# Kernel optimization log

Hardware: AMD Instinct MI355X
Metric: run time of the kernel (lower is better)

The kernel has to match this reference:

```python
import jax, jax.numpy as jnp
import numpy as np


def _conv(x, w):
    # NCHW cross-correlation, stride 1, zero 'SAME' padding (kernel//2 each side)
    return jax.lax.conv_general_dilated(x, w, window_strides=(1, 1), padding='SAME',
                                        dimension_numbers=('NCHW', 'OIHW', 'NCHW'))


def _conv_t(y, w):
    # adjoint of _conv(x, w): spatially flipped kernel with in/out channels swapped
    wt = jnp.transpose(jnp.flip(w, (2, 3)), (1, 0, 2, 3))
    return _conv(y, wt)


def _spline(x, coefs, x_min, x_max):
    # uniform-knot linear spline with linear extrapolation (clamp=False)
    K = coefs.shape[-1]
    step = (x_max - x_min) / (K - 1)
    t = (x - x_min) / step
    idx = jnp.clip(jnp.floor(t), 0, K - 2).astype(jnp.int32)
    frac = t - idx
    if coefs.shape[0] == 1:
        c = coefs[0]
        c0, c1v = c[idx], c[idx + 1]
    else:
        ch = jnp.arange(coefs.shape[0]).reshape(1, -1, 1, 1)
        c0, c1v = coefs[ch, idx], coefs[ch, idx + 1]
    return c0 * (1.0 - frac) + c1v * frac


def _forward(y, sigma, w1_0, w1_1, w1_2, m1_0, m1_1, m1_2, m2_w, m3_w,
             c_sp1, c_sp2, c_sp3, c_lam, c_scal, n_out, n_in):
    LC = m2_w.shape[0]  # last_c = 128
    lmbda = _spline(sigma, c_lam, -1.0, 51.0)              # (B,1,1,1)
    sig_e = sigma * jnp.ones((1, LC, 1, 1), sigma.dtype)   # (B,LC,1,1)
    scaling = jnp.exp(_spline(sig_e, c_scal, -1.0, 51.0)) / (sig_e + 1e-5)

    def W1(x):
        return _conv(_conv(_conv(x, w1_0), w1_1), w1_2)

    def W1t(v):
        return _conv_t(_conv_t(_conv_t(v, w1_2), w1_1), w1_0)

    def cal_mask(x):
        t = _spline(jnp.abs(_conv(_conv(_conv(x, m1_0), m1_1), m1_2)), c_sp1, 0.0, 3.0)
        t = _spline(jnp.abs(_conv(t, m2_w)), c_sp2, 0.0, 3.0)
        t = _conv(t, m3_w)
        t = _spline(scaling * jnp.abs(t), c_sp3, 0.0, 3.0)  # last_act
        return jnp.clip(t, 0.01, 1.0)

    def BtB(x, mask):
        # (x + lmbda * Lt(L(x))) / (1 + lmbda) with L(x)=W1(x)*mask, Lt(v)=W1t(v*mask)
        return (x + lmbda * W1t(W1(x) * mask * mask)) / (1.0 + lmbda)

    eps_in = 1e-6

    def cg(bb, x0, mask):
        # masked-batch CG: converged images (r_norm <= eps) get alpha=beta=0,
        # mathematically identical to the torch code's dynamic batch shrinking
        b = bb / (1.0 + lmbda)
        r0 = b - BtB(x0, mask)
        rn0 = jnp.sum(r0 * r0, axis=(1, 2, 3), keepdims=True)

        def step(carry, _):
            x, r, p, rn = carry
            act = rn > eps_in
            Bp = BtB(p, mask)
            denom = jnp.sum(p * Bp, axis=(1, 2, 3), keepdims=True)
            alpha = jnp.where(act, rn / jnp.where(act, denom, 1.0), 0.0)
            x = x + alpha * p
            r2 = r - alpha * Bp
            rn2 = jnp.sum(r2 * r2, axis=(1, 2, 3), keepdims=True)
            beta = jnp.where(act, rn2 / jnp.where(act, rn, 1.0), 0.0)
            return (x, r2, r2 + beta * p, rn2), None

        (x, _, _, _), _ = jax.lax.scan(step, (x0, r0, r0, rn0), None, length=n_in)
        return x

    # eval-mode denoise: outer mask-recompute loop around inner CG solves
    c_k = jnp.zeros_like(y)
    c_k_old = c_k
    for _ in range(n_out):
        mask = cal_mask(c_k)
        c_k = cg(y, c_k_old, mask)
        c_k_old = c_k
    return c_k


def setup_inputs() -> dict:
    key = jax.random.key(0)
    ks = jax.random.split(key, 10)
    B, H, W = 8, 128, 128
    y = jax.random.normal(ks[0], (B, 1, H, W), jnp.float32)
    sigma = jax.random.uniform(ks[1], (B, 1, 1, 1), jnp.float32) * 0.2 + 0.05

    def cw(k, co, ci, ksz):
        return jax.random.normal(k, (co, ci, ksz, ksz), jnp.float32) / np.float32(np.sqrt(ci * ksz * ksz))

    w1_0 = cw(ks[2], 4, 1, 9); w1_1 = cw(ks[3], 8, 4, 9); w1_2 = cw(ks[4], 128, 8, 9)
    m1_0 = cw(ks[5], 4, 1, 9); m1_1 = cw(ks[6], 8, 4, 9); m1_2 = cw(ks[7], 128, 8, 9)
    m2_w = cw(ks[8], 128, 128, 3); m3_w = cw(ks[9], 128, 128, 3)
    c_sp1 = jnp.linspace(0.0, 3.0, 31).astype(jnp.float32).reshape(1, 31)   # identity init
    c_sp2 = jnp.linspace(0.0, 3.0, 31).astype(jnp.float32).reshape(1, 31)   # identity init
    g = jnp.linspace(0.0, 3.0, 31).astype(jnp.float32)
    c_sp3 = jnp.exp(-(g - 1.5) ** 2).reshape(1, 31)                          # gaussian init
    c_lam = jnp.linspace(-1.0, 51.0, 53).astype(jnp.float32).reshape(1, 53)  # identity init
    c_scal = 3.0 * jnp.ones((128, 14), jnp.float32)                          # constant 3.0 init
    return {"y": y, "sigma": sigma,
            "w1_0": w1_0, "w1_1": w1_1, "w1_2": w1_2,
            "m1_0": m1_0, "m1_1": m1_1, "m1_2": m1_2,
            "m2_w": m2_w, "m3_w": m3_w,
            "c_sp1": c_sp1, "c_sp2": c_sp2, "c_sp3": c_sp3,
            "c_lam": c_lam, "c_scal": c_scal,
            "n_out": 2, "n_in": 6}


def reference(y, sigma, w1_0, w1_1, w1_2, m1_0, m1_1, m1_2, m2_w, m3_w,
              c_sp1, c_sp2, c_sp3, c_lam, c_scal, n_out, n_in):
    return _forward(y, sigma, w1_0, w1_1, w1_2, m1_0, m1_1, m1_2, m2_w, m3_w,
                    c_sp1, c_sp2, c_sp3, c_lam, c_scal, n_out, n_in)
```

## Files before the change

kernel.cpp:

```cpp
#include <hip/hip_runtime.h>

#define HW 16384
#define BATCH 8

typedef unsigned short u16;
typedef __attribute__((ext_vector_type(8))) short bfrag;
typedef __attribute__((ext_vector_type(4))) float ffrag;
typedef __attribute__((ext_vector_type(4))) float f4v;

__device__ __forceinline__ u16 f2bf(float f) {
  unsigned int u = __float_as_uint(f);
  u += 0x7FFFu + ((u >> 16) & 1u);
  return (u16)(u >> 16);
}
__device__ __forceinline__ float bf2f(u16 h) {
  return __uint_as_float(((unsigned int)h) << 16);
}
__device__ __forceinline__ ffrag mfma16(bfrag a, bfrag b, ffrag c) {
  return __builtin_amdgcn_mfma_f32_16x16x32_bf16(a, b, c, 0, 0, 0);
}

__device__ __forceinline__ float spline_eval(float x, const float* __restrict__ c,
                                             int K, float xmin, float xmax) {
  float step = (xmax - xmin) / (float)(K - 1);
  float t = (x - xmin) / step;
  float fidx = floorf(t);
  fidx = fminf(fmaxf(fidx, 0.0f), (float)(K - 2));
  int idx = (int)fidx;
  float frac = t - fidx;
  return c[idx] * (1.0f - frac) + c[idx + 1] * frac;
}
__device__ __forceinline__ float spline31(float x, const float* __restrict__ c) {
  float t = x * 10.0f;
  float fi = floorf(t);
  fi = fminf(fmaxf(fi, 0.0f), 29.0f);
  int i = (int)fi;
  float fr = t - fi;
  return c[i] * (1.0f - fr) + c[i + 1] * fr;
}

template<int KS, int CIW, int CO, int NTT, int NSLICE, int TAPS, int CHUNKS, bool TR>
__global__ void k_prepw(const float* __restrict__ W, u16* __restrict__ hi,
                        u16* __restrict__ lo) {
  int gid = blockIdx.x * 256 + threadIdx.x;
  const int total = NSLICE * CHUNKS * NTT * 64;
  if (gid >= total) return;
  int L = gid & 63;
  int rest = gid >> 6;
  int ntg = rest % NTT; rest /= NTT;
  int ch = rest % CHUNKS;
  int sl = rest / CHUNKS;
  int q = L >> 4, n = L & 15;
  int tap = ch * 4 + q;
  int co = ntg * 16 + n;
  int dh = tap / KS, dw = tap - dh * KS;
  for (int j = 0; j < 8; ++j) {
    int ci = sl * 8 + j;
    float v = 0.0f;
    if (tap < TAPS && co < CO) {
      if (TR)
        v = W[(((size_t)ci * CO + co) * KS + (KS - 1 - dh)) * KS + (KS - 1 - dw)];
      else
        v = W[(((size_t)co * CIW + ci) * KS + dh) * KS + dw];
    }
    u16 h = f2bf(v);
    hi[(size_t)gid * 8 + j] = h;
    lo[(size_t)gid * 8 + j] = f2bf(v - bf2f(h));
  }
}

template<int KS, int SLICES, int TAPS, int CHUNKS, int NT, int NTT, int EPI>
__global__ __launch_bounds__(256) void bconv(
    const u16* __restrict__ in, const u16* __restrict__ wHi,
    float* __restrict__ outF, u16* __restrict__ outBf,
    const u16* __restrict__ mskc)
{
  constexpr int P  = KS / 2;
  constexpr int IW = 16 + 2 * P;
  constexpr int IH = 16 + 2 * P;

  __shared__ __align__(16) u16 sA[IH * IW * 8];

  const int tid = threadIdx.x;
  const int wv  = tid >> 6;
  const int L   = tid & 63;
  const int q   = L >> 4;
  const int n16 = L & 15;

  const int tx = blockIdx.x & 7, ty = blockIdx.x >> 3;
  const int w0 = tx * 16, h0 = ty * 16;
  const int bb = blockIdx.y;
  const int bz = blockIdx.z;

  ffrag acc[4][NT];
#pragma unroll
  for (int i = 0; i < 4; ++i)
#pragma unroll
    for (int t = 0; t < NT; ++t) acc[i][t] = (ffrag)0.0f;

  for (int slc = 0; slc < SLICES; ++slc) {
    __syncthreads();
    for (int e = tid; e < IH * IW; e += 256) {
      int ih = e / IW, iw = e - ih * IW;
      int gh = h0 + ih - P, gw = w0 + iw - P;
      f4v v = (f4v)0.0f;
      if (gh >= 0 && gh < 128 && gw >= 0 && gw < 128)
        v = *(const f4v*)(in + (((size_t)(bb * SLICES + slc) * HW) + gh * 128 + gw) * 8);
      *(f4v*)(sA + (size_t)e * 8) = v;
    }
    __syncthreads();

    const u16* wS = wHi + (size_t)slc * CHUNKS * NTT * 512;
    for (int ch = 0; ch < CHUNKS; ++ch) {
      int tap = ch * 4 + q;
      int dh = 0, dw = 0;
      if (tap < TAPS) { dh = tap / KS; dw = tap - dh * KS; }
      int toff = dh * IW + dw;
      bfrag A[4];
#pragma unroll
      for (int i = 0; i < 4; ++i)
        A[i] = *(const bfrag*)(sA + ((wv * 4 + i) * IW + n16 + toff) * 8);
#pragma unroll
      for (int t = 0; t < NT; ++t) {
        bfrag B = *(const bfrag*)(wS + ((size_t)ch * NTT + bz * NT + t) * 512 + L * 8);
#pragma unroll
        for (int i = 0; i < 4; ++i) acc[i][t] = mfma16(A[i], B, acc[i][t]);
      }
    }
  }

#pragma unroll
  for (int i = 0; i < 4; ++i) {
    const int h = h0 + wv * 4 + i;
#pragma unroll
    for (int t = 0; t < NT; ++t) {
      const int co = bz * (NT * 16) + t * 16 + n16;
#pragma unroll
      for (int r = 0; r < 4; ++r) {
        const int w = w0 + q * 4 + r;
        float v = acc[i][t][r];
        if (EPI == 0) {
          if (n16 < 8)
            outF[(((size_t)bb * 8 + n16) * 128 + h) * 128 + w] = v;
        } else if (EPI == 3) {
          size_t o = (((size_t)(bb * 16 + (co >> 3)) * HW) + h * 128 + w) * 8 + (co & 7);
          float m = bf2f(mskc[o]);
          outBf[o] = f2bf(v * m * m);
        }
      }
    }
  }
}

template<int KS, int CIN, int NSLICE, int TAPS, int CHUNKS,
         int TH, int MTW, int NT, int NTT, int EPI>
__global__ __launch_bounds__(256) void mconv(
    const float* __restrict__ inF,
    const u16* __restrict__ wHi, const u16* __restrict__ wLo,
    float* __restrict__ outF, u16* __restrict__ outBf,
    const float* __restrict__ sp, const float* __restrict__ sl,
    int binOfs, int boutOfs)
{
  constexpr int P  = KS / 2;
  constexpr int IW = 16 + 2 * P;
  constexpr int IH = TH + 2 * P;

  __shared__ __align__(16) u16 sHi[IH * IW * 8];
  __shared__ __align__(16) u16 sLo[IH * IW * 8];

  const int tid = threadIdx.x;
  const int wv  = tid >> 6;
  const int L   = tid & 63;
  const int q   = L >> 4;
  const int n16 = L & 15;

  const int tx = blockIdx.x & 7;
  const int ty = blockIdx.x >> 3;
  const int w0 = tx * 16, h0 = ty * TH;
  const int bin  = (int)blockIdx.y + binOfs;
  const int bout = (int)blockIdx.y + boutOfs;
  const int bz = blockIdx.z;

  ffrag acc[MTW][NT];
#pragma unroll
  for (int i = 0; i < MTW; ++i)
#pragma unroll
    for (int t = 0; t < NT; ++t) acc[i][t] = (ffrag)0.0f;

  for (int slc = 0; slc < NSLICE; ++slc) {
    __syncthreads();
    for (int e = tid; e < IH * IW; e += 256) {
      int ih = e / IW, iw = e - ih * IW;
      int gh = h0 + ih - P, gw = w0 + iw - P;
      float v[8];
      if (gh >= 0 && gh < 128 && gw >= 0 && gw < 128) {
        const float* s = inF + (((size_t)(bin * 128 + gh) * 128 + gw) * CIN + slc * 8);
        f4v a = *(const f4v*)s;
        f4v b2 = *(const f4v*)(s + 4);
        v[0] = a[0]; v[1] = a[1]; v[2] = a[2]; v[3] = a[3];
        v[4] = b2[0]; v[5] = b2[1]; v[6] = b2[2]; v[7] = b2[3];
      } else {
#pragma unroll
        for (int j = 0; j < 8; ++j) v[j] = 0.0f;
      }
#pragma unroll
      for (int j = 0; j < 8; ++j) {
        u16 hb = f2bf(v[j]);
        sHi[e * 8 + j] = hb;
        sLo[e * 8 + j] = f2bf(v[j] - bf2f(hb));
      }
    }
    __syncthreads();

    const u16* wHs = wHi + (size_t)slc * CHUNKS * NTT * 512;
    const u16* wLs = wLo + (size_t)slc * CHUNKS * NTT * 512;
    for (int ch = 0; ch < CHUNKS; ++ch) {
      int tap = ch * 4 + q;
      int dh = tap / KS;
      int dw = tap - dh * KS;
      int toff = (tap < TAPS) ? (dh * IW + dw) : 0;
      bfrag Ah[MTW], Al[MTW];
#pragma unroll
      for (int i = 0; i < MTW; ++i) {
        int a8 = ((wv * MTW + i) * IW + n16 + toff) * 8;
        Ah[i] = *(const bfrag*)(sHi + a8);
        Al[i] = *(const bfrag*)(sLo + a8);
      }
#pragma unroll
      for (int t = 0; t < NT; ++t) {
        size_t off = ((size_t)ch * NTT + bz * NT + t) * 512 + L * 8;
        bfrag Bh = *(const bfrag*)(wHs + off);
        bfrag Bl = *(const bfrag*)(wLs + off);
#pragma unroll
        for (int i = 0; i < MTW; ++i) {
          acc[i][t] = mfma16(Ah[i], Bh, acc[i][t]);
          acc[i][t] = mfma16(Ah[i], Bl, acc[i][t]);
          acc[i][t] = mfma16(Al[i], Bh, acc[i][t]);
        }
      }
    }
  }

#pragma unroll
  for (int i = 0; i < MTW; ++i) {
    const int h = h0 + wv * MTW + i;
#pragma unroll
    for (int t = 0; t < NT; ++t) {
      const int co = bz * (NT * 16) + t * 16 + n16;
#pragma unroll
      for (int r = 0; r < 4; ++r) {
        const int w = w0 + q * 4 + r;
        float v = acc[i][t][r];
        if (EPI == 1) {
          outF[(((size_t)bout * 128 + h) * 128 + w) * 128 + co] = spline31(fabsf(v), sp);
        } else if (EPI == 2) {
          float s = sl[bout * 128 + co];
          float x = spline31(s * fabsf(v), sp);
          x = fminf(fmaxf(x, 0.01f), 1.0f);
          size_t o = (((size_t)(bout * 16 + (co >> 3)) * HW) + h * 128 + w) * 8 + (co & 7);
          outBf[o] = f2bf(x);
        }
      }
    }
  }
}

template<int OUT>
__global__ __launch_bounds__(256) void fused_fwd(
    const float* __restrict__ in, const float* __restrict__ wA,
    const float* __restrict__ wB, float* __restrict__ outF,
    u16* __restrict__ outBf)
{
  __shared__ float sX[32 * 48];
  __shared__ float sT4[4][24 * 41];
  __shared__ float sWA[81 * 4];
  __shared__ float sWB[4 * 81 * 8];

  const int tid = threadIdx.x;
  const int b   = blockIdx.z;
  const int h0  = (blockIdx.x >> 2) * 16;
  const int w0  = (blockIdx.x & 3) * 32;

  for (int e = tid; e < 32 * 48; e += 256) {
    int r = e / 48, c = e - r * 48;
    int gh = h0 - 8 + r, gw = w0 - 8 + c;
    float v = 0.0f;
    if (gh >= 0 && gh < 128 && gw >= 0 && gw < 128)
      v = in[(size_t)b * HW + gh * 128 + gw];
    sX[e] = v;
  }
  for (int e = tid; e < 324; e += 256) {
    int co = e & 3, tap = e >> 2;
    sWA[tap * 4 + co] = wA[co * 81 + tap];
  }
  for (int e = tid; e < 2592; e += 256) {
    int co = e & 7;
    int rest = e >> 3;
    int tap = rest % 81, ci = rest / 81;
    sWB[(ci * 81 + tap) * 8 + co] = wB[((size_t)co * 4 + ci) * 81 + tap];
  }
  __syncthreads();

  for (int e = tid; e < 960; e += 256) {
    int r = e / 40, c = e - r * 40;
    int gh = h0 - 4 + r, gw = w0 - 4 + c;
    float a0 = 0.0f, a1 = 0.0f, a2 = 0.0f, a3 = 0.0f;
    if (gh >= 0 && gh < 128 && gw >= 0 && gw < 128) {
      for (int kh = 0; kh < 9; ++kh) {
#pragma unroll
        for (int kw = 0; kw < 9; ++kw) {
          float x = sX[(r + kh) * 48 + (c + kw)];
          const float* wp = &sWA[(kh * 9 + kw) * 4];
          a0 += x * wp[0]; a1 += x * wp[1]; a2 += x * wp[2]; a3 += x * wp[3];
        }
      }
    }
    sT4[0][r * 41 + c] = a0;
    sT4[1][r * 41 + c] = a1;
    sT4[2][r * 41 + c] = a2;
    sT4[3][r * 41 + c] = a3;
  }
  __syncthreads();

  const int c  = tid & 31;
  const int r0 = tid >> 5;
  float acc[2][8];
#pragma unroll
  for (int j = 0; j < 2; ++j)
#pragma unroll
    for (int co = 0; co < 8; ++co) acc[j][co] = 0.0f;

  for (int ci = 0; ci < 4; ++ci) {
    const float* t4c = sT4[ci];
    for (int kh = 0; kh < 9; ++kh) {
#pragma unroll
      for (int kw = 0; kw < 9; ++kw) {
        float x0 = t4c[(r0 + kh) * 41 + c + kw];
        float x1 = t4c[(r0 + 8 + kh) * 41 + c + kw];
        const float* wp = &sWB[(ci * 81 + kh * 9 + kw) * 8];
#pragma unroll
        for (int co = 0; co < 8; ++co) {
          acc[0][co] += x0 * wp[co];
          acc[1][co] += x1 * wp[co];
        }
      }
    }
  }

#pragma unroll
  for (int j = 0; j < 2; ++j) {
    const int h = h0 + r0 + 8 * j;
    const int w = w0 + c;
#pragma unroll
    for (int co = 0; co < 8; ++co) {
      float v = acc[j][co];
      if (OUT == 0)
        outF[(((size_t)b * 128 + h) * 128 + w) * 8 + co] = v;
      else
        outBf[((size_t)b * HW + h * 128 + w) * 8 + co] = f2bf(v);
    }
  }
}

template<int KS, int CI, int CO, int CIC, int COT, int TH, int EPI, bool TR>
__global__ __launch_bounds__(256) void conv_k(
    const float* __restrict__ in, const float* __restrict__ wt,
    float* __restrict__ out, const float* __restrict__ aux,
    const float* __restrict__ sl)
{
  constexpr int P  = KS / 2;
  constexpr int TW = 32;
  constexpr int IH = TH + 2 * P;
  constexpr int IW = TW + 2 * P;
  constexpr int RPT = TH / 8;
  constexpr int NCH = CI / CIC;
  static_assert(CIC * NCH == CI, "channel split mismatch");

  __shared__ float sIn[CIC * IH * IW];
  __shared__ float sW[CIC * KS * KS * COT];

  const int tid = threadIdx.x;
  const int nTW = 128 / TW;
  const int th0 = (blockIdx.x / nTW) * TH;
  const int tw0 = (blockIdx.x % nTW) * TW;
  const int b   = blockIdx.z;

  float acc[RPT][COT];
#pragma unroll
  for (int j = 0; j < RPT; ++j)
#pragma unroll
    for (int co = 0; co < COT; ++co) acc[j][co] = 0.0f;

  const int c  = tid & 31;
  const int r0 = tid >> 5;

  for (int ch = 0; ch < NCH; ++ch) {
    const int ci0 = ch * CIC;
    __syncthreads();
    for (int e = tid; e < CIC * IH * IW; e += 256) {
      int ci  = e / (IH * IW);
      int rem = e - ci * (IH * IW);
      int ih  = rem / IW;
      int iw  = rem - ih * IW;
      int gh = th0 + ih - P, gw = tw0 + iw - P;
      float v = 0.0f;
      if (gh >= 0 && gh < 128 && gw >= 0 && gw < 128)
        v = in[((size_t)(b * CI + ci0 + ci) * 128 + gh) * 128 + gw];
      sIn[e] = v;
    }
    for (int e = tid; e < CIC * KS * KS * COT; e += 256) {
      int co = e & (COT - 1);
      int k  = e / COT;
      int ci = k / (KS * KS);
      int kk = k - ci * (KS * KS);
      int kh = kk / KS, kw = kk - kh * KS;
      float wv;
      if (!TR)
        wv = wt[(((size_t)co * CI + ci0 + ci) * KS + kh) * KS + kw];
      else
        wv = wt[(((size_t)(ci0 + ci) * CO + co) * KS + (KS - 1 - kh)) * KS + (KS - 1 - kw)];
      sW[e] = wv;
    }
    __syncthreads();

    for (int ci = 0; ci < CIC; ++ci) {
      for (int kh = 0; kh < KS; ++kh) {
        const float* inb = &sIn[(ci * IH + r0 + kh) * IW + c];
        const float* wb  = &sW[(ci * KS + kh) * KS * COT];
#pragma unroll
        for (int kw = 0; kw < KS; ++kw) {
          float xv[RPT];
#pragma unroll
          for (int j = 0; j < RPT; ++j) xv[j] = inb[8 * j * IW + kw];
#pragma unroll
          for (int co = 0; co < COT; ++co) {
            float wv = wb[kw * COT + co];
#pragma unroll
            for (int j = 0; j < RPT; ++j) acc[j][co] += xv[j] * wv;
          }
        }
      }
    }
  }

#pragma unroll
  for (int j = 0; j < RPT; ++j) {
    const int h = th0 + r0 + 8 * j;
    const int w = tw0 + c;
#pragma unroll
    for (int co = 0; co < COT; ++co) {
      float v = acc[j][co];
      if (EPI == 5) {
        size_t o = ((size_t)b * 128 + h) * 128 + w;
        float l = sl[b];
        out[o] = (aux[o] + l * v) / (1.0f + l);
      } else {
        out[((size_t)(b * CO + co) * 128 + h) * 128 + w] = v;
      }
    }
  }
}

__global__ void k_scalars(const float* __restrict__ sigma, const float* __restrict__ c_lam,
                          const float* __restrict__ c_scal, float* __restrict__ lam,
                          float* __restrict__ scal) {
  int tid = threadIdx.x;
  if (tid < BATCH) lam[tid] = spline_eval(sigma[tid], c_lam, 53, -1.0f, 51.0f);
  for (int j = tid; j < BATCH * 128; j += 256) {
    int b = j >> 7, chn = j & 127;
    float s = sigma[b];
    scal[j] = expf(spline_eval(s, c_scal + chn * 14, 14, -1.0f, 51.0f)) / (s + 1e-5f);
  }
}

__global__ void k_binit(const float* __restrict__ y, const float* __restrict__ lam,
                        float* __restrict__ bimg, float* __restrict__ x) {
  int i = blockIdx.x * 256 + threadIdx.x;
  int b = i >> 14;
  bimg[i] = y[i] / (1.0f + lam[b]);
  x[i] = 0.0f;
}

__global__ void k_rinit(const float* __restrict__ bimg, const float* __restrict__ Bp,
                        float* __restrict__ r, float* __restrict__ p) {
  int i = blockIdx.x * 256 + threadIdx.x;
  float v = bimg[i] - Bp[i];
  r[i] = v;
  p[i] = v;
}

__global__ void k_dot(const float* __restrict__ a, const float* __restrict__ bv,
                      float* __restrict__ out) {
  __shared__ float s[256];
  int b = blockIdx.x;
  float sum = 0.0f;
  for (int i = threadIdx.x; i < HW; i += 256) sum += a[b * HW + i] * bv[b * HW + i];
  s[threadIdx.x] = sum;
  __syncthreads();
  for (int st = 128; st > 0; st >>= 1) {
    if (threadIdx.x < st) s[threadIdx.x] += s[threadIdx.x + st];
    __syncthreads();
  }
  if (threadIdx.x == 0) out[b] = s[0];
}

__global__ void k_update_xr(float* __restrict__ x, float* __restrict__ r,
                            const float* __restrict__ p, const float* __restrict__ Bp,
                            const float* __restrict__ rn, const float* __restrict__ den) {
  int i = blockIdx.x * 256 + threadIdx.x;
  int b = i >> 14;
  float rnb = rn[b];
  float alpha = rnb > 1e-6f ? rnb / den[b] : 0.0f;
  x[i] += alpha * p[i];
  r[i] -= alpha * Bp[i];
}

__global__ void k_update_p(float* __restrict__ p, const float* __restrict__ r,
                           const float* __restrict__ rnOld, const float* __restrict__ rnNew) {
  int i = blockIdx.x * 256 + threadIdx.x;
  int b = i >> 14;
  float ro = rnOld[b];
  float beta = ro > 1e-6f ? rnNew[b] / ro : 0.0f;
  p[i] = r[i] + beta * p[i];
}

__global__ void k_copy(const float* __restrict__ x, float* __restrict__ out) {
  int i = blockIdx.x * 256 + threadIdx.x;
  out[i] = x[i];
}

extern "C" void kernel_launch(void* const* d_in, const int* in_sizes, int n_in_,
                              void* d_out, int out_size, void* d_ws, size_t ws_size,
                              hipStream_t stream) {
  const float* y      = (const float*)d_in[0];
  const float* sigma  = (const float*)d_in[1];
  const float* w1_0   = (const float*)d_in[2];
  const float* w1_1   = (const float*)d_in[3];
  const float* w1_2   = (const float*)d_in[4];
  const float* m1_0   = (const float*)d_in[5];
  const float* m1_1   = (const float*)d_in[6];
  const float* m1_2   = (const float*)d_in[7];
  const float* m2_w   = (const float*)d_in[8];
  const float* m3_w   = (const float*)d_in[9];
  const float* c_sp1  = (const float*)d_in[10];
  const float* c_sp2  = (const float*)d_in[11];
  const float* c_sp3  = (const float*)d_in[12];
  const float* c_lam  = (const float*)d_in[13];
  const float* c_scal = (const float*)d_in[14];

  char* cur = (char*)d_ws;
  auto alloc = [&](size_t bytes) {
    char* p = cur;
    cur += (bytes + 255) & ~(size_t)255;
    return p;
  };

  u16* wA_hi  = (u16*)alloc(86016 * 2);
  u16* wA_lo  = (u16*)alloc(86016 * 2);
  u16* wAm_hi = (u16*)alloc(86016 * 2);
  u16* wAm_lo = (u16*)alloc(86016 * 2);
  u16* wB_hi  = (u16*)alloc(172032 * 2);
  u16* wB_lo  = (u16*)alloc(172032 * 2);
  u16* wC2_hi = (u16*)alloc(196608 * 2);
  u16* wC2_lo = (u16*)alloc(196608 * 2);
  u16* wC3_hi = (u16*)alloc(196608 * 2);
  u16* wC3_lo = (u16*)alloc(196608 * 2);

  char* region1 = alloc((size_t)16777216 * 4);
  float* P1f    = (float*)region1;
  u16*   big2c  = (u16*)region1;
  u16* mask_c = (u16*)alloc((size_t)16777216 * 2);
  char* region2 = alloc((size_t)4 * 128 * 128 * 128 * 4);
  float* P2s = (float*)region2;
  float* t8n = (float*)region2;
  float* t4  = (float*)(region2 + 4194304);
  char* region3 = alloc((size_t)1048576 * 4);
  float* t8f = (float*)region3;
  u16*   t8c = (u16*)region3;

  float* bimg = (float*)alloc(131072 * 4);
  float* xbuf = (float*)alloc(131072 * 4);
  float* rbuf = (float*)alloc(131072 * 4);
  float* pbuf = (float*)alloc(131072 * 4);
  float* Bp   = (float*)alloc(131072 * 4);
  float* lam  = (float*)alloc(8 * 4);
  float* scal = (float*)alloc(1024 * 4);
  float* rnA  = (float*)alloc(8 * 4);
  float* rnB  = (float*)alloc(8 * 4);
  float* den  = (float*)alloc(8 * 4);

  const dim3 blk(256);

  k_prepw<9, 8, 128, 8, 1, 81, 21, false><<<dim3(42), blk, 0, stream>>>(w1_2, wA_hi, wA_lo);
  k_prepw<9, 8, 128, 8, 1, 81, 21, false><<<dim3(42), blk, 0, stream>>>(m1_2, wAm_hi, wAm_lo);
  k_prepw<9, 8, 8, 1, 16, 81, 21, true><<<dim3(84), blk, 0, stream>>>(w1_2, wB_hi, wB_lo);
  k_prepw<3, 128, 128, 8, 16, 9, 3, false><<<dim3(96), blk, 0, stream>>>(m2_w, wC2_hi, wC2_lo);
  k_prepw<3, 128, 128, 8, 16, 9, 3, false><<<dim3(96), blk, 0, stream>>>(m3_w, wC3_hi, wC3_lo);

  k_scalars<<<dim3(1), blk, 0, stream>>>(sigma, c_lam, c_scal, lam, scal);
  k_binit<<<dim3(512), blk, 0, stream>>>(y, lam, bimg, xbuf);

  auto BtB = [&](const float* vin, float* vout) {
    fused_fwd<1><<<dim3(32, 1, 8), blk, 0, stream>>>(vin, w1_0, w1_1, nullptr, t8c);
    bconv<9, 1, 81, 21, 2, 8, 3><<<dim3(64, 8, 4), blk, 0, stream>>>(
        t8c, wA_hi, nullptr, big2c, mask_c);
    bconv<9, 16, 81, 21, 1, 1, 0><<<dim3(64, 8, 1), blk, 0, stream>>>(
        big2c, wB_hi, t8n, nullptr, nullptr);
    conv_k<9, 8, 4, 2, 4, 16, 0, true><<<dim3(32, 1, 8), blk, 0, stream>>>(
        t8n, w1_1, t4, nullptr, nullptr);
    conv_k<9, 4, 1, 1, 1, 16, 5, true><<<dim3(32, 1, 8), blk, 0, stream>>>(
        t4, w1_0, vout, vin, lam);
  };

  for (int outer = 0; outer < 2; ++outer) {
    fused_fwd<0><<<dim3(32, 1, 8), blk, 0, stream>>>(xbuf, m1_0, m1_1, t8f, nullptr);
    mconv<9, 8, 1, 81, 21, 16, 4, 2, 8, 1><<<dim3(64, 8, 4), blk, 0, stream>>>(
        t8f, wAm_hi, wAm_lo, P1f, nullptr, c_sp1, nullptr, 0, 0);
    for (int bc = 0; bc < 2; ++bc) {
      mconv<3, 128, 16, 9, 3, 16, 4, 2, 8, 1><<<dim3(64, 4, 4), blk, 0, stream>>>(
          P1f, wC2_hi, wC2_lo, P2s, nullptr, c_sp2, nullptr, bc * 4, 0);
      mconv<3, 128, 16, 9, 3, 16, 4, 2, 8, 2><<<dim3(64, 4, 4), blk, 0, stream>>>(
          P2s, wC3_hi, wC3_lo, nullptr, mask_c, c_sp3, scal, 0, bc * 4);
    }

    BtB(xbuf, Bp);
    k_rinit<<<dim3(512), blk, 0, stream>>>(bimg, Bp, rbuf, pbuf);
    k_dot<<<dim3(8), blk, 0, stream>>>(rbuf, rbuf, rnA);

    float* rA = rnA;
    float* rB = rnB;
    for (int it = 0; it < 6; ++it) {
      BtB(pbuf, Bp);
      k_dot<<<dim3(8), blk, 0, stream>>>(pbuf, Bp, den);
      k_update_xr<<<dim3(512), blk, 0, stream>>>(xbuf, rbuf, pbuf, Bp, rA, den);
      k_dot<<<dim3(8), blk, 0, stream>>>(rbuf, rbuf, rB);
      k_update_p<<<dim3(512), blk, 0, stream>>>(pbuf, rbuf, rA, rB);
      float* tmp = rA; rA = rB; rB = tmp;
    }
  }

  k_copy<<<dim3(512), blk, 0, stream>>>(xbuf, (float*)d_out);
}
```

Measured before the change: 3.433 ms.

## Fuse transposed conv tail and CG vector updates into fewer kernels

Replaces the two fp32 transposed 9x9 conv kernels (8->4 and 4->1 channels) with a single fused_tail kernel. It keeps the 4-channel intermediate, with halo, in shared memory and applies the lambda blend in its epilogue. The preceding bconv now writes a bf16 channel-interleaved 8-channel output instead of fp32 planar, which halves that traffic but adds bf16 rounding. The CG residual init, x/r update, norm and p update are merged into per-image kernels with in-block reductions. This cuts launches and global round trips, but those kernels now run on only 8 blocks, and fused_tail recomputes the halo region.

```diff
diff --git a/kernel.cpp b/kernel.cpp
--- a/kernel.cpp
+++ b/kernel.cpp
@@ -72,8 +72,7 @@
 template<int KS, int SLICES, int TAPS, int CHUNKS, int NT, int NTT, int EPI>
 __global__ __launch_bounds__(256) void bconv(
     const u16* __restrict__ in, const u16* __restrict__ wHi,
-    float* __restrict__ outF, u16* __restrict__ outBf,
-    const u16* __restrict__ mskc)
+    u16* __restrict__ outBf, const u16* __restrict__ mskc)
 {
   constexpr int P  = KS / 2;
   constexpr int IW = 16 + 2 * P;
@@ -139,9 +138,9 @@
       for (int r = 0; r < 4; ++r) {
         const int w = w0 + q * 4 + r;
         float v = acc[i][t][r];
-        if (EPI == 0) {
+        if (EPI == 4) {
           if (n16 < 8)
-            outF[(((size_t)bb * 8 + n16) * 128 + h) * 128 + w] = v;
+            outBf[((size_t)bb * HW + h * 128 + w) * 8 + n16] = f2bf(v);
         } else if (EPI == 3) {
           size_t o = (((size_t)(bb * 16 + (co >> 3)) * HW) + h * 128 + w) * 8 + (co & 7);
           float m = bf2f(mskc[o]);
@@ -362,102 +361,92 @@
   }
 }
 
-template<int KS, int CI, int CO, int CIC, int COT, int TH, int EPI, bool TR>
-__global__ __launch_bounds__(256) void conv_k(
-    const float* __restrict__ in, const float* __restrict__ wt,
-    float* __restrict__ out, const float* __restrict__ aux,
-    const float* __restrict__ sl)
+__global__ __launch_bounds__(256) void fused_tail(
+    const u16* __restrict__ t8v, const float* __restrict__ w11,
+    const float* __restrict__ w10, const float* __restrict__ vin,
+    const float* __restrict__ lam, float* __restrict__ vout)
 {
-  constexpr int P  = KS / 2;
-  constexpr int TW = 32;
-  constexpr int IH = TH + 2 * P;
-  constexpr int IW = TW + 2 * P;
-  constexpr int RPT = TH / 8;
-  constexpr int NCH = CI / CIC;
-  static_assert(CIC * NCH == CI, "channel split mismatch");
-
-  __shared__ float sIn[CIC * IH * IW];
-  __shared__ float sW[CIC * KS * KS * COT];
+  __shared__ float sX[8][32 * 33];
+  __shared__ float sT4[4][24 * 25];
+  __shared__ float sW1[8 * 81 * 4];
+  __shared__ float sW0[4 * 81];
 
   const int tid = threadIdx.x;
-  const int nTW = 128 / TW;
-  const int th0 = (blockIdx.x / nTW) * TH;
-  const int tw0 = (blockIdx.x % nTW) * TW;
   const int b   = blockIdx.z;
-
-  float acc[RPT][COT];
-#pragma unroll
-  for (int j = 0; j < RPT; ++j)
-#pragma unroll
-    for (int co = 0; co < COT; ++co) acc[j][co] = 0.0f;
-
-  const int c  = tid & 31;
-  const int r0 = tid >> 5;
-
-  for (int ch = 0; ch < NCH; ++ch) {
-    const int ci0 = ch * CIC;
-    __syncthreads();
-    for (int e = tid; e < CIC * IH * IW; e += 256) {
-      int ci  = e / (IH * IW);
-      int rem = e - ci * (IH * IW);
-      int ih  = rem / IW;
-      int iw  = rem - ih * IW;
-      int gh = th0 + ih - P, gw = tw0 + iw - P;
-      float v = 0.0f;
-      if (gh >= 0 && gh < 128 && gw >= 0 && gw < 128)
-        v = in[((size_t)(b * CI + ci0 + ci) * 128 + gh) * 128 + gw];
-      sIn[e] = v;
-    }
-    for (int e = tid; e < CIC * KS * KS * COT; e += 256) {
-      int co = e & (COT - 1);
-      int k  = e / COT;
-      int ci = k / (KS * KS);
-      int kk = k - ci * (KS * KS);
-      int kh = kk / KS, kw = kk - kh * KS;
-      float wv;
-      if (!TR)
-        wv = wt[(((size_t)co * CI + ci0 + ci) * KS + kh) * KS + kw];
-      else
-        wv = wt[(((size_t)(ci0 + ci) * CO + co) * KS + (KS - 1 - kh)) * KS + (KS - 1 - kw)];
-      sW[e] = wv;
-    }
-    __syncthreads();
-
-    for (int ci = 0; ci < CIC; ++ci) {
-      for (int kh = 0; kh < KS; ++kh) {
-        const float* inb = &sIn[(ci * IH + r0 + kh) * IW + c];
-        const float* wb  = &sW[(ci * KS + kh) * KS * COT];
-#pragma unroll
-        for (int kw = 0; kw < KS; ++kw) {
-          float xv[RPT];
-#pragma unroll
-          for (int j = 0; j < RPT; ++j) xv[j] = inb[8 * j * IW + kw];
-#pragma unroll
-          for (int co = 0; co < COT; ++co) {
-            float wv = wb[kw * COT + co];
-#pragma unroll
-            for (int j = 0; j < RPT; ++j) acc[j][co] += xv[j] * wv;
+  const int h0  = (blockIdx.x >> 3) * 16;
+  const int w0  = (blockIdx.x & 7) * 16;
+
+  for (int e = tid; e < 1024; e += 256) {
+    int r = e >> 5, c = e & 31;
+    int gh = h0 - 8 + r, gw = w0 - 8 + c;
+    float v[8];
+    if (gh >= 0 && gh < 128 && gw >= 0 && gw < 128) {
+      const u16* s = t8v + ((size_t)b * HW + gh * 128 + gw) * 8;
+#pragma unroll
+      for (int ci = 0; ci < 8; ++ci) v[ci] = bf2f(s[ci]);
+    } else {
+#pragma unroll
+      for (int ci = 0; ci < 8; ++ci) v[ci] = 0.0f;
+    }
+#pragma unroll
+    for (int ci = 0; ci < 8; ++ci) sX[ci][r * 33 + c] = v[ci];
+  }
+  for (int e = tid; e < 2592; e += 256) {
+    int co = e & 3;
+    int rest = e >> 2;
+    int tap = rest % 81, ci = rest / 81;
+    sW1[(ci * 81 + tap) * 4 + co] = w11[(size_t)(ci * 4 + co) * 81 + (80 - tap)];
+  }
+  for (int e = tid; e < 324; e += 256) {
+    int tap = e % 81, ci = e / 81;
+    sW0[ci * 81 + tap] = w10[(size_t)ci * 81 + (80 - tap)];
+  }
+  __syncthreads();
+
+  for (int e = tid; e < 288; e += 256) {
+    int r = e / 12, c2 = (e - r * 12) * 2;
+    int gh = h0 - 4 + r;
+    int gw0 = w0 - 4 + c2;
+    float a0[4] = {0, 0, 0, 0}, a1[4] = {0, 0, 0, 0};
+    for (int ci = 0; ci < 8; ++ci) {
+      for (int kh = 0; kh < 9; ++kh) {
+        const float* xb = &sX[ci][(r + kh) * 33 + c2];
+#pragma unroll
+        for (int kw = 0; kw < 9; ++kw) {
+          float x0 = xb[kw], x1 = xb[kw + 1];
+          const float* wp = &sW1[(ci * 81 + kh * 9 + kw) * 4];
+#pragma unroll
+          for (int co = 0; co < 4; ++co) {
+            a0[co] += x0 * wp[co];
+            a1[co] += x1 * wp[co];
           }
         }
       }
     }
-  }
-
-#pragma unroll
-  for (int j = 0; j < RPT; ++j) {
-    const int h = th0 + r0 + 8 * j;
-    const int w = tw0 + c;
-#pragma unroll
-    for (int co = 0; co < COT; ++co) {
-      float v = acc[j][co];
-      if (EPI == 5) {
-        size_t o = ((size_t)b * 128 + h) * 128 + w;
-        float l = sl[b];
-        out[o] = (aux[o] + l * v) / (1.0f + l);
-      } else {
-        out[((size_t)(b * CO + co) * 128 + h) * 128 + w] = v;
-      }
-    }
+    bool in0 = (gh >= 0 && gh < 128 && gw0 >= 0 && gw0 < 128);
+    bool in1 = (gh >= 0 && gh < 128 && (gw0 + 1) >= 0 && (gw0 + 1) < 128);
+#pragma unroll
+    for (int co = 0; co < 4; ++co) {
+      sT4[co][r * 25 + c2]     = in0 ? a0[co] : 0.0f;
+      sT4[co][r * 25 + c2 + 1] = in1 ? a1[co] : 0.0f;
+    }
+  }
+  __syncthreads();
+
+  {
+    int r = tid >> 4, c = tid & 15;
+    float acc = 0.0f;
+    for (int ci = 0; ci < 4; ++ci) {
+      for (int kh = 0; kh < 9; ++kh) {
+        const float* xb = &sT4[ci][(r + kh) * 25 + c];
+        const float* wp = &sW0[ci * 81 + kh * 9];
+#pragma unroll
+        for (int kw = 0; kw < 9; ++kw) acc += xb[kw] * wp[kw];
+      }
+    }
+    size_t o = (size_t)b * HW + (h0 + r) * 128 + (w0 + c);
+    float l = lam[b];
+    vout[o] = (vin[o] + l * acc) / (1.0f + l);
   }
 }
 
@@ -479,14 +468,6 @@
   int b = i >> 14;
   bimg[i] = y[i] / (1.0f + lam[b]);
   x[i] = 0.0f;
-}
-
-__global__ void k_rinit(const float* __restrict__ bimg, const float* __restrict__ Bp,
-                        float* __restrict__ r, float* __restrict__ p) {
-  int i = blockIdx.x * 256 + threadIdx.x;
-  float v = bimg[i] - Bp[i];
-  r[i] = v;
-  p[i] = v;
 }
 
 __global__ void k_dot(const float* __restrict__ a, const float* __restrict__ bv,
@@ -504,24 +485,56 @@
   if (threadIdx.x == 0) out[b] = s[0];
 }
 
-__global__ void k_update_xr(float* __restrict__ x, float* __restrict__ r,
-                            const float* __restrict__ p, const float* __restrict__ Bp,
-                            const float* __restrict__ rn, const float* __restrict__ den) {
-  int i = blockIdx.x * 256 + threadIdx.x;
-  int b = i >> 14;
+__global__ void k_cg0(const float* __restrict__ bimg, const float* __restrict__ Bp,
+                      float* __restrict__ r, float* __restrict__ p,
+                      float* __restrict__ rn) {
+  __shared__ float s[256];
+  int b = blockIdx.x;
+  size_t base = (size_t)b << 14;
+  float local = 0.0f;
+  for (int i = threadIdx.x; i < HW; i += 256) {
+    float v = bimg[base + i] - Bp[base + i];
+    r[base + i] = v;
+    p[base + i] = v;
+    local += v * v;
+  }
+  s[threadIdx.x] = local;
+  __syncthreads();
+  for (int st = 128; st > 0; st >>= 1) {
+    if (threadIdx.x < st) s[threadIdx.x] += s[threadIdx.x + st];
+    __syncthreads();
+  }
+  if (threadIdx.x == 0) rn[b] = s[0];
+}
+
+__global__ void k_cg2(float* __restrict__ x, float* __restrict__ r,
+                      float* __restrict__ p, const float* __restrict__ Bp,
+                      float* __restrict__ rn, const float* __restrict__ den) {
+  __shared__ float s[256];
+  int b = blockIdx.x;
+  size_t base = (size_t)b << 14;
   float rnb = rn[b];
-  float alpha = rnb > 1e-6f ? rnb / den[b] : 0.0f;
-  x[i] += alpha * p[i];
-  r[i] -= alpha * Bp[i];
-}
-
-__global__ void k_update_p(float* __restrict__ p, const float* __restrict__ r,
-                           const float* __restrict__ rnOld, const float* __restrict__ rnNew) {
-  int i = blockIdx.x * 256 + threadIdx.x;
-  int b = i >> 14;
-  float ro = rnOld[b];
-  float beta = ro > 1e-6f ? rnNew[b] / ro : 0.0f;
-  p[i] = r[i] + beta * p[i];
+  bool act = rnb > 1e-6f;
+  float alpha = act ? rnb / den[b] : 0.0f;
+  float local = 0.0f;
+  for (int i = threadIdx.x; i < HW; i += 256) {
+    float pv = p[base + i];
+    x[base + i] += alpha * pv;
+    float rr = r[base + i] - alpha * Bp[base + i];
+    r[base + i] = rr;
+    local += rr * rr;
+  }
+  s[threadIdx.x] = local;
+  __syncthreads();
+  for (int st = 128; st > 0; st >>= 1) {
+    if (threadIdx.x < st) s[threadIdx.x] += s[threadIdx.x + st];
+    __syncthreads();
+  }
+  float rn2 = s[0];
+  float beta = act ? rn2 / rnb : 0.0f;
+  if (threadIdx.x == 0) rn[b] = rn2;
+  for (int i = threadIdx.x; i < HW; i += 256)
+    p[base + i] = r[base + i] + beta * p[base + i];
 }
 
 __global__ void k_copy(const float* __restrict__ x, float* __restrict__ out) {
@@ -567,13 +580,12 @@
   u16* wC3_lo = (u16*)alloc(196608 * 2);
 
   char* region1 = alloc((size_t)16777216 * 4);
-  float* P1f    = (float*)region1;
-  u16*   big2c  = (u16*)region1;
+  float* P1f   = (float*)region1;
+  u16*   big2c = (u16*)region1;
   u16* mask_c = (u16*)alloc((size_t)16777216 * 2);
   char* region2 = alloc((size_t)4 * 128 * 128 * 128 * 4);
   float* P2s = (float*)region2;
-  float* t8n = (float*)region2;
-  float* t4  = (float*)(region2 + 4194304);
+  u16*   t8v = (u16*)region2;
   char* region3 = alloc((size_t)1048576 * 4);
   float* t8f = (float*)region3;
   u16*   t8c = (u16*)region3;
@@ -585,8 +597,7 @@
   float* Bp   = (float*)alloc(131072 * 4);
   float* lam  = (float*)alloc(8 * 4);
   float* scal = (float*)alloc(1024 * 4);
-  float* rnA  = (float*)alloc(8 * 4);
-  float* rnB  = (float*)alloc(8 * 4);
+  float* rn   = (float*)alloc(8 * 4);
   float* den  = (float*)alloc(8 * 4);
 
   const dim3 blk(256);
@@ -603,13 +614,10 @@
   auto BtB = [&](const float* vin, float* vout) {
     fused_fwd<1><<<dim3(32, 1, 8), blk, 0, stream>>>(vin, w1_0, w1_1, nullptr, t8c);
     bconv<9, 1, 81, 21, 2, 8, 3><<<dim3(64, 8, 4), blk, 0, stream>>>(
-        t8c, wA_hi, nullptr, big2c, mask_c);
-    bconv<9, 16, 81, 21, 1, 1, 0><<<dim3(64, 8, 1), blk, 0, stream>>>(
-        big2c, wB_hi, t8n, nullptr, nullptr);
-    conv_k<9, 8, 4, 2, 4, 16, 0, true><<<dim3(32, 1, 8), blk, 0, stream>>>(
-        t8n, w1_1, t4, nullptr, nullptr);
-    conv_k<9, 4, 1, 1, 1, 16, 5, true><<<dim3(32, 1, 8), blk, 0, stream>>>(
-        t4, w1_0, vout, vin, lam);
+        t8c, wA_hi, big2c, mask_c);
+    bconv<9, 16, 81, 21, 1, 1, 4><<<dim3(64, 8, 1), blk, 0, stream>>>(
+        big2c, wB_hi, t8v, nullptr);
+    fused_tail<<<dim3(64, 1, 8), blk, 0, stream>>>(t8v, w1_1, w1_0, vin, lam, vout);
   };
 
   for (int outer = 0; outer < 2; ++outer) {
@@ -624,18 +632,12 @@
     }
 
     BtB(xbuf, Bp);
-    k_rinit<<<dim3(512), blk, 0, stream>>>(bimg, Bp, rbuf, pbuf);
-    k_dot<<<dim3(8), blk, 0, stream>>>(rbuf, rbuf, rnA);
-
-    float* rA = rnA;
-    float* rB = rnB;
+    k_cg0<<<dim3(8), blk, 0, stream>>>(bimg, Bp, rbuf, pbuf, rn);
+
     for (int it = 0; it < 6; ++it) {
       BtB(pbuf, Bp);
       k_dot<<<dim3(8), blk, 0, stream>>>(pbuf, Bp, den);
-      k_update_xr<<<dim3(512), blk, 0, stream>>>(xbuf, rbuf, pbuf, Bp, rA, den);
-      k_dot<<<dim3(8), blk, 0, stream>>>(rbuf, rbuf, rB);
-      k_update_p<<<dim3(512), blk, 0, stream>>>(pbuf, rbuf, rA, rB);
-      float* tmp = rA; rA = rB; rB = tmp;
+      k_cg2<<<dim3(8), blk, 0, stream>>>(xbuf, rbuf, pbuf, Bp, rn, den);
     }
   }
 
```

New measurement: 3.536 ms. 1.03x slower.

## Store mask-path activations as pre-split bf16 hi/lo and fuse CG updates

Applied to the files above, without the earlier changes.

Intermediate activations feeding the MFMA mask convolutions are now written in channel-blocked bf16 hi/lo pairs by the producer epilogues, so the consumer staging loops just copy vectors instead of converting fp32 and splitting per load. Separately, the CG residual init, x/r update, norm reduction and p update are fused into per-batch kernels, removing several launches and the final copy. The fused CG kernels use only one block per image, which reduces parallelism for the elementwise work.

```diff
diff --git a/kernel.cpp b/kernel.cpp
--- a/kernel.cpp
+++ b/kernel.cpp
@@ -155,9 +155,9 @@
 template<int KS, int CIN, int NSLICE, int TAPS, int CHUNKS,
          int TH, int MTW, int NT, int NTT, int EPI>
 __global__ __launch_bounds__(256) void mconv(
-    const float* __restrict__ inF,
+    const u16* __restrict__ inHi, const u16* __restrict__ inLo,
     const u16* __restrict__ wHi, const u16* __restrict__ wLo,
-    float* __restrict__ outF, u16* __restrict__ outBf,
+    u16* __restrict__ outHi, u16* __restrict__ outLo,
     const float* __restrict__ sp, const float* __restrict__ sl,
     int binOfs, int boutOfs)
 {
@@ -192,23 +192,14 @@
     for (int e = tid; e < IH * IW; e += 256) {
       int ih = e / IW, iw = e - ih * IW;
       int gh = h0 + ih - P, gw = w0 + iw - P;
-      float v[8];
+      f4v vh = (f4v)0.0f, vl = (f4v)0.0f;
       if (gh >= 0 && gh < 128 && gw >= 0 && gw < 128) {
-        const float* s = inF + (((size_t)(bin * 128 + gh) * 128 + gw) * CIN + slc * 8);
-        f4v a = *(const f4v*)s;
-        f4v b2 = *(const f4v*)(s + 4);
-        v[0] = a[0]; v[1] = a[1]; v[2] = a[2]; v[3] = a[3];
-        v[4] = b2[0]; v[5] = b2[1]; v[6] = b2[2]; v[7] = b2[3];
-      } else {
-#pragma unroll
-        for (int j = 0; j < 8; ++j) v[j] = 0.0f;
-      }
-#pragma unroll
-      for (int j = 0; j < 8; ++j) {
-        u16 hb = f2bf(v[j]);
-        sHi[e * 8 + j] = hb;
-        sLo[e * 8 + j] = f2bf(v[j] - bf2f(hb));
-      }
+        size_t g = (((size_t)(bin * (CIN / 8) + slc) * HW) + gh * 128 + gw) * 8;
+        vh = *(const f4v*)(inHi + g);
+        vl = *(const f4v*)(inLo + g);
+      }
+      *(f4v*)(sHi + (size_t)e * 8) = vh;
+      *(f4v*)(sLo + (size_t)e * 8) = vl;
     }
     __syncthreads();
 
@@ -251,14 +242,17 @@
       for (int r = 0; r < 4; ++r) {
         const int w = w0 + q * 4 + r;
         float v = acc[i][t][r];
+        size_t o = (((size_t)(bout * 16 + (co >> 3)) * HW) + h * 128 + w) * 8 + (co & 7);
         if (EPI == 1) {
-          outF[(((size_t)bout * 128 + h) * 128 + w) * 128 + co] = spline31(fabsf(v), sp);
+          float x = spline31(fabsf(v), sp);
+          u16 hb = f2bf(x);
+          outHi[o] = hb;
+          outLo[o] = f2bf(x - bf2f(hb));
         } else if (EPI == 2) {
           float s = sl[bout * 128 + co];
           float x = spline31(s * fabsf(v), sp);
           x = fminf(fmaxf(x, 0.01f), 1.0f);
-          size_t o = (((size_t)(bout * 16 + (co >> 3)) * HW) + h * 128 + w) * 8 + (co & 7);
-          outBf[o] = f2bf(x);
+          outHi[o] = f2bf(x);
         }
       }
     }
@@ -268,8 +262,8 @@
 template<int OUT>
 __global__ __launch_bounds__(256) void fused_fwd(
     const float* __restrict__ in, const float* __restrict__ wA,
-    const float* __restrict__ wB, float* __restrict__ outF,
-    u16* __restrict__ outBf)
+    const float* __restrict__ wB, u16* __restrict__ oHi,
+    u16* __restrict__ oLo)
 {
   __shared__ float sX[32 * 48];
   __shared__ float sT4[4][24 * 41];
@@ -354,10 +348,14 @@
 #pragma unroll
     for (int co = 0; co < 8; ++co) {
       float v = acc[j][co];
-      if (OUT == 0)
-        outF[(((size_t)b * 128 + h) * 128 + w) * 8 + co] = v;
-      else
-        outBf[((size_t)b * HW + h * 128 + w) * 8 + co] = f2bf(v);
+      size_t o = ((size_t)b * HW + h * 128 + w) * 8 + co;
+      if (OUT == 0) {
+        u16 hb = f2bf(v);
+        oHi[o] = hb;
+        oLo[o] = f2bf(v - bf2f(hb));
+      } else {
+        oHi[o] = f2bf(v);
+      }
     }
   }
 }
@@ -481,14 +479,6 @@
   x[i] = 0.0f;
 }
 
-__global__ void k_rinit(const float* __restrict__ bimg, const float* __restrict__ Bp,
-                        float* __restrict__ r, float* __restrict__ p) {
-  int i = blockIdx.x * 256 + threadIdx.x;
-  float v = bimg[i] - Bp[i];
-  r[i] = v;
-  p[i] = v;
-}
-
 __global__ void k_dot(const float* __restrict__ a, const float* __restrict__ bv,
                       float* __restrict__ out) {
   __shared__ float s[256];
@@ -504,29 +494,59 @@
   if (threadIdx.x == 0) out[b] = s[0];
 }
 
-__global__ void k_update_xr(float* __restrict__ x, float* __restrict__ r,
-                            const float* __restrict__ p, const float* __restrict__ Bp,
-                            const float* __restrict__ rn, const float* __restrict__ den) {
-  int i = blockIdx.x * 256 + threadIdx.x;
-  int b = i >> 14;
+__global__ void k_cg0(const float* __restrict__ bimg, const float* __restrict__ Bp,
+                      float* __restrict__ r, float* __restrict__ p,
+                      float* __restrict__ rn) {
+  __shared__ float s[256];
+  int b = blockIdx.x;
+  size_t base = (size_t)b << 14;
+  float local = 0.0f;
+  for (int i = threadIdx.x; i < HW; i += 256) {
+    float v = bimg[base + i] - Bp[base + i];
+    r[base + i] = v;
+    p[base + i] = v;
+    local += v * v;
+  }
+  s[threadIdx.x] = local;
+  __syncthreads();
+  for (int st = 128; st > 0; st >>= 1) {
+    if (threadIdx.x < st) s[threadIdx.x] += s[threadIdx.x + st];
+    __syncthreads();
+  }
+  if (threadIdx.x == 0) rn[b] = s[0];
+}
+
+__global__ void k_cg2(float* __restrict__ x, float* __restrict__ r,
+                      float* __restrict__ p, const float* __restrict__ Bp,
+                      float* __restrict__ rn, const float* __restrict__ den,
+                      float* __restrict__ xout) {
+  __shared__ float s[256];
+  int b = blockIdx.x;
+  size_t base = (size_t)b << 14;
   float rnb = rn[b];
-  float alpha = rnb > 1e-6f ? rnb / den[b] : 0.0f;
-  x[i] += alpha * p[i];
-  r[i] -= alpha * Bp[i];
-}
-
-__global__ void k_update_p(float* __restrict__ p, const float* __restrict__ r,
-                           const float* __restrict__ rnOld, const float* __restrict__ rnNew) {
-  int i = blockIdx.x * 256 + threadIdx.x;
-  int b = i >> 14;
-  float ro = rnOld[b];
-  float beta = ro > 1e-6f ? rnNew[b] / ro : 0.0f;
-  p[i] = r[i] + beta * p[i];
-}
-
-__global__ void k_copy(const float* __restrict__ x, float* __restrict__ out) {
-  int i = blockIdx.x * 256 + threadIdx.x;
-  out[i] = x[i];
+  bool act = rnb > 1e-6f;
+  float alpha = act ? rnb / den[b] : 0.0f;
+  float local = 0.0f;
+  for (int i = threadIdx.x; i < HW; i += 256) {
+    float pv = p[base + i];
+    float xv = x[base + i] + alpha * pv;
+    x[base + i] = xv;
+    if (xout) xout[base + i] = xv;
+    float rr = r[base + i] - alpha * Bp[base + i];
+    r[base + i] = rr;
+    local += rr * rr;
+  }
+  s[threadIdx.x] = local;
+  __syncthreads();
+  for (int st = 128; st > 0; st >>= 1) {
+    if (threadIdx.x < st) s[threadIdx.x] += s[threadIdx.x + st];
+    __syncthreads();
+  }
+  float rn2 = s[0];
+  float beta = act ? rn2 / rnb : 0.0f;
+  if (threadIdx.x == 0) rn[b] = rn2;
+  for (int i = threadIdx.x; i < HW; i += 256)
+    p[base + i] = r[base + i] + beta * p[base + i];
 }
 
 extern "C" void kernel_launch(void* const* d_in, const int* in_sizes, int n_in_,
@@ -566,17 +586,20 @@
   u16* wC3_hi = (u16*)alloc(196608 * 2);
   u16* wC3_lo = (u16*)alloc(196608 * 2);
 
-  char* region1 = alloc((size_t)16777216 * 4);
-  float* P1f    = (float*)region1;
-  u16*   big2c  = (u16*)region1;
+  char* region1 = alloc((size_t)16777216 * 2 * 2);
+  u16* P1hi  = (u16*)region1;
+  u16* P1lo  = (u16*)(region1 + (size_t)16777216 * 2);
+  u16* big2c = (u16*)region1;
   u16* mask_c = (u16*)alloc((size_t)16777216 * 2);
-  char* region2 = alloc((size_t)4 * 128 * 128 * 128 * 4);
-  float* P2s = (float*)region2;
+  char* region2 = alloc((size_t)8388608 * 2 * 2);
+  u16* P2hi = (u16*)region2;
+  u16* P2lo = (u16*)(region2 + (size_t)8388608 * 2);
   float* t8n = (float*)region2;
-  float* t4  = (float*)(region2 + 4194304);
-  char* region3 = alloc((size_t)1048576 * 4);
-  float* t8f = (float*)region3;
-  u16*   t8c = (u16*)region3;
+  float* t4  = (float*)(region2 + (size_t)4194304 * 4);
+  char* region3 = alloc((size_t)1048576 * 2 * 2);
+  u16* t8hi = (u16*)region3;
+  u16* t8lo = (u16*)(region3 + (size_t)1048576 * 2);
+  u16* t8c  = (u16*)region3;
 
   float* bimg = (float*)alloc(131072 * 4);
   float* xbuf = (float*)alloc(131072 * 4);
@@ -585,8 +608,7 @@
   float* Bp   = (float*)alloc(131072 * 4);
   float* lam  = (float*)alloc(8 * 4);
   float* scal = (float*)alloc(1024 * 4);
-  float* rnA  = (float*)alloc(8 * 4);
-  float* rnB  = (float*)alloc(8 * 4);
+  float* rn   = (float*)alloc(8 * 4);
   float* den  = (float*)alloc(8 * 4);
 
   const dim3 blk(256);
@@ -601,7 +623,7 @@
   k_binit<<<dim3(512), blk, 0, stream>>>(y, lam, bimg, xbuf);
 
   auto BtB = [&](const float* vin, float* vout) {
-    fused_fwd<1><<<dim3(32, 1, 8), blk, 0, stream>>>(vin, w1_0, w1_1, nullptr, t8c);
+    fused_fwd<1><<<dim3(32, 1, 8), blk, 0, stream>>>(vin, w1_0, w1_1, t8c, nullptr);
     bconv<9, 1, 81, 21, 2, 8, 3><<<dim3(64, 8, 4), blk, 0, stream>>>(
         t8c, wA_hi, nullptr, big2c, mask_c);
     bconv<9, 16, 81, 21, 1, 1, 0><<<dim3(64, 8, 1), blk, 0, stream>>>(
@@ -613,31 +635,24 @@
   };
 
   for (int outer = 0; outer < 2; ++outer) {
-    fused_fwd<0><<<dim3(32, 1, 8), blk, 0, stream>>>(xbuf, m1_0, m1_1, t8f, nullptr);
+    fused_fwd<0><<<dim3(32, 1, 8), blk, 0, stream>>>(xbuf, m1_0, m1_1, t8hi, t8lo);
     mconv<9, 8, 1, 81, 21, 16, 4, 2, 8, 1><<<dim3(64, 8, 4), blk, 0, stream>>>(
-        t8f, wAm_hi, wAm_lo, P1f, nullptr, c_sp1, nullptr, 0, 0);
+        t8hi, t8lo, wAm_hi, wAm_lo, P1hi, P1lo, c_sp1, nullptr, 0, 0);
     for (int bc = 0; bc < 2; ++bc) {
       mconv<3, 128, 16, 9, 3, 16, 4, 2, 8, 1><<<dim3(64, 4, 4), blk, 0, stream>>>(
-          P1f, wC2_hi, wC2_lo, P2s, nullptr, c_sp2, nullptr, bc * 4, 0);
+          P1hi, P1lo, wC2_hi, wC2_lo, P2hi, P2lo, c_sp2, nullptr, bc * 4, 0);
       mconv<3, 128, 16, 9, 3, 16, 4, 2, 8, 2><<<dim3(64, 4, 4), blk, 0, stream>>>(
-          P2s, wC3_hi, wC3_lo, nullptr, mask_c, c_sp3, scal, 0, bc * 4);
+          P2hi, P2lo, wC3_hi, wC3_lo, mask_c, nullptr, c_sp3, scal, 0, bc * 4);
     }
 
     BtB(xbuf, Bp);
-    k_rinit<<<dim3(512), blk, 0, stream>>>(bimg, Bp, rbuf, pbuf);
-    k_dot<<<dim3(8), blk, 0, stream>>>(rbuf, rbuf, rnA);
-
-    float* rA = rnA;
-    float* rB = rnB;
+    k_cg0<<<dim3(8), blk, 0, stream>>>(bimg, Bp, rbuf, pbuf, rn);
+
     for (int it = 0; it < 6; ++it) {
       BtB(pbuf, Bp);
       k_dot<<<dim3(8), blk, 0, stream>>>(pbuf, Bp, den);
-      k_update_xr<<<dim3(512), blk, 0, stream>>>(xbuf, rbuf, pbuf, Bp, rA, den);
-      k_dot<<<dim3(8), blk, 0, stream>>>(rbuf, rbuf, rB);
-      k_update_p<<<dim3(512), blk, 0, stream>>>(pbuf, rbuf, rA, rB);
-      float* tmp = rA; rA = rB; rB = tmp;
-    }
-  }
-
-  k_copy<<<dim3(512), blk, 0, stream>>>(xbuf, (float*)d_out);
-}
+      float* xout = (outer == 1 && it == 5) ? (float*)d_out : nullptr;
+      k_cg2<<<dim3(8), blk, 0, stream>>>(xbuf, rbuf, pbuf, Bp, rn, den, xout);
+    }
+  }
+}
```

After: 3.656 ms. 6.5% more time.
